# Optimization experiments

Measured on AMD Instinct MI355X. Metric: run time of the kernel, lower is better.

Reference implementation:

```python
import jax, jax.numpy as jnp
import numpy as np

B, Lq, Lk, E = 4, 512, 512, 128
D = 2 * E  # input feature dim = 2*encode_size


def setup_inputs() -> dict:
    key = jax.random.key(0)
    ks = jax.random.split(key, 6)
    return {
        "query": jax.random.normal(ks[0], (B, Lq, D), jnp.float32),
        "key": jax.random.normal(ks[1], (B, Lk, D), jnp.float32),
        "value": jax.random.normal(ks[2], (B, Lq, D), jnp.float32),
        "Wc1": jax.random.normal(ks[3], (D, E), jnp.float32) / np.sqrt(D),
        "Wc2": jax.random.normal(ks[4], (D, E), jnp.float32) / np.sqrt(D),
        "vc": jax.random.normal(ks[5], (E,), jnp.float32) / np.sqrt(E),
    }


def reference(query, key, value, Wc1, Wc2, vc):
    # q: [B, Lq, E], k: [B, Lk, E]
    q = query @ Wc1
    k = key @ Wc2
    # additive (Bahdanau) scores: tanh(q + k) reduced by vc -> [B, Lk, Lq]
    sjt = jnp.einsum('blqe,e->blq', jnp.tanh(q[:, None, :, :] + k[:, :, None, :]), vc)
    atten = jax.nn.softmax(sjt, axis=2)  # softmax over Lq (dim=2), dropout p=0.0 is identity
    context = jnp.einsum('blq,bqd->bld', atten, value)  # [B, Lk, D]
    return (context, atten)
```

## Files before the change

kernel.cpp:

```cpp
#include <hip/hip_runtime.h>

#define NB 4
#define LQ 512
#define LK 512
#define EE 128
#define DD 256

__device__ __forceinline__ float fast_rcp(float x) { return __builtin_amdgcn_rcpf(x); }

__global__ __launch_bounds__(256) void proj_exp_kernel(
    const float* __restrict__ query, const float* __restrict__ key,
    const float* __restrict__ Wc1, const float* __restrict__ Wc2,
    float* __restrict__ EqT, float* __restrict__ Ek)
{
    __shared__ float in_s[8][DD];
    const int r0 = blockIdx.x * 8;
    const bool is_q = (r0 < NB * LQ);
    const float* src = is_q ? query : key;
    const float* W   = is_q ? Wc1   : Wc2;
    const int rbase  = is_q ? r0    : r0 - NB * LQ;

    const float4* srow4 = (const float4*)(src + (size_t)rbase * DD);
    #pragma unroll
    for (int i = 0; i < 2; ++i)
        ((float4*)in_s)[i * 256 + threadIdx.x] = srow4[i * 256 + threadIdx.x];
    __syncthreads();

    const int c  = threadIdx.x & 127;
    const int rg = threadIdx.x >> 7;
    float acc[4] = {0.f, 0.f, 0.f, 0.f};
    for (int d = 0; d < DD; d += 8) {
        const float w0 = W[(d + 0) * EE + c];
        const float w1 = W[(d + 1) * EE + c];
        const float w2 = W[(d + 2) * EE + c];
        const float w3 = W[(d + 3) * EE + c];
        const float w4 = W[(d + 4) * EE + c];
        const float w5 = W[(d + 5) * EE + c];
        const float w6 = W[(d + 6) * EE + c];
        const float w7 = W[(d + 7) * EE + c];
        #pragma unroll
        for (int i = 0; i < 4; ++i) {
            const float4 xa = *(const float4*)&in_s[rg * 4 + i][d];
            const float4 xb = *(const float4*)&in_s[rg * 4 + i][d + 4];
            acc[i] += xa.x * w0 + xa.y * w1 + xa.z * w2 + xa.w * w3
                    + xb.x * w4 + xb.y * w5 + xb.z * w6 + xb.w * w7;
        }
    }
    if (is_q) {
        const int b    = rbase >> 9;
        const int qloc = (rbase & 511) + rg * 4;
        float4 o;
        o.x = __expf(2.0f * acc[0]); o.y = __expf(2.0f * acc[1]);
        o.z = __expf(2.0f * acc[2]); o.w = __expf(2.0f * acc[3]);
        *(float4*)&EqT[((size_t)(b * EE + c)) * LQ + qloc] = o;
    } else {
        #pragma unroll
        for (int i = 0; i < 4; ++i)
            Ek[(size_t)(rbase + rg * 4 + i) * EE + c] = __expf(2.0f * acc[i]);
    }
}

__global__ __launch_bounds__(512) void atten_kernel(
    const float* __restrict__ EqT, const float* __restrict__ Ek,
    const float* __restrict__ vc, float* __restrict__ attn)
{
    __shared__ float  ek_s[4][EE];
    __shared__ float  vc_s[EE];
    __shared__ float  s2p_s[3][4][LQ];
    __shared__ float  sj_s[4][LQ];
    __shared__ float2 mZ_s[4][2];
    __shared__ float  scale_s[4][2];
    const int b   = blockIdx.x >> 7;
    const int lt  = blockIdx.x & 127;
    const int l0  = lt * 4;
    const int tid = threadIdx.x;
    const int qq  = tid & 127;
    const int eg  = tid >> 7;

    ((float*)ek_s)[tid] = Ek[((size_t)b * LK + l0) * EE + tid];
    if (tid < EE) vc_s[tid] = vc[tid];
    __syncthreads();

    float vcsum = 0.f;
    #pragma unroll
    for (int e = 0; e < EE; e += 4) {
        const float4 v = *(const float4*)&vc_s[e];
        vcsum += (v.x + v.y) + (v.z + v.w);
    }

    const float4* eq4 = (const float4*)(EqT + (size_t)b * EE * LQ);
    float s2[4][4];
    #pragma unroll
    for (int l = 0; l < 4; ++l) { s2[l][0]=0.f; s2[l][1]=0.f; s2[l][2]=0.f; s2[l][3]=0.f; }

    #pragma unroll 4
    for (int i = 0; i < 32; ++i) {
        const int e = eg * 32 + i;
        const float4 a  = eq4[(size_t)e * 128 + qq];
        const float  vv = vc_s[e];
        #pragma unroll
        for (int l = 0; l < 4; ++l) {
            const float kk = ek_s[l][e];
            s2[l][0] += vv * fast_rcp(a.x * kk + 1.0f);
            s2[l][1] += vv * fast_rcp(a.y * kk + 1.0f);
            s2[l][2] += vv * fast_rcp(a.z * kk + 1.0f);
            s2[l][3] += vv * fast_rcp(a.w * kk + 1.0f);
        }
    }

    if (eg > 0) {
        #pragma unroll
        for (int l = 0; l < 4; ++l)
            *(float4*)&s2p_s[eg - 1][l][qq * 4] =
                make_float4(s2[l][0], s2[l][1], s2[l][2], s2[l][3]);
    }
    __syncthreads();
    if (eg == 0) {
        #pragma unroll
        for (int l = 0; l < 4; ++l) {
            const float4 p0 = *(const float4*)&s2p_s[0][l][qq * 4];
            const float4 p1 = *(const float4*)&s2p_s[1][l][qq * 4];
            const float4 p2 = *(const float4*)&s2p_s[2][l][qq * 4];
            float4 sj;
            sj.x = vcsum - 2.0f * (s2[l][0] + p0.x + p1.x + p2.x);
            sj.y = vcsum - 2.0f * (s2[l][1] + p0.y + p1.y + p2.y);
            sj.z = vcsum - 2.0f * (s2[l][2] + p0.z + p1.z + p2.z);
            sj.w = vcsum - 2.0f * (s2[l][3] + p0.w + p1.w + p2.w);
            *(float4*)&sj_s[l][qq * 4] = sj;
        }
    }
    __syncthreads();

    const int w = tid >> 6, lane = tid & 63;
    const int l = w & 3, h2 = w >> 2, base = h2 * 256;
    float m = -1e30f;
    #pragma unroll
    for (int i = 0; i < 4; ++i) m = fmaxf(m, sj_s[l][base + lane + 64 * i]);
    #pragma unroll
    for (int off = 32; off >= 1; off >>= 1) m = fmaxf(m, __shfl_xor(m, off));
    float Z = 0.f;
    #pragma unroll
    for (int i = 0; i < 4; ++i) {
        const int idx = base + lane + 64 * i;
        const float ex = __expf(sj_s[l][idx] - m);
        sj_s[l][idx] = ex;
        Z += ex;
    }
    #pragma unroll
    for (int off = 32; off >= 1; off >>= 1) Z += __shfl_xor(Z, off);
    if (lane == 0) mZ_s[l][h2] = make_float2(m, Z);
    __syncthreads();
    if (lane == 0) {
        const float2 A = mZ_s[l][0], B2 = mZ_s[l][1];
        const float M  = fmaxf(A.x, B2.x);
        const float Zt = A.y * __expf(A.x - M) + B2.y * __expf(B2.x - M);
        scale_s[l][h2] = __expf((h2 ? B2.x : A.x) - M) * fast_rcp(Zt);
    }
    __syncthreads();

    const int q = tid;
    #pragma unroll
    for (int li = 0; li < 4; ++li)
        attn[(size_t)(b * LK + l0 + li) * LQ + q] = sj_s[li][q] * scale_s[li][q >> 8];
}

__global__ __launch_bounds__(1024) void context_kernel(
    const float* __restrict__ attn, const float* __restrict__ value,
    float* __restrict__ ctx)
{
    const int b    = blockIdx.x >> 6;
    const int lt   = blockIdx.x & 63;
    const int row0 = b * LK + lt * 8;
    const int tid  = threadIdx.x;
    const int g    = tid >> 6;
    const int lane = tid & 63;
    const float4* v4 = (const float4*)(value + (size_t)b * LQ * DD);

    float4 ac[8];
    #pragma unroll
    for (int l = 0; l < 8; ++l) ac[l] = make_float4(0.f, 0.f, 0.f, 0.f);

    const int q0 = g * 32;
    for (int q = q0; q < q0 + 32; q += 4) {
        float4 a[8];
        #pragma unroll
        for (int l = 0; l < 8; ++l)
            a[l] = *(const float4*)(attn + (size_t)(row0 + l) * LQ + q);
        const float4 v0 = v4[(size_t)(q + 0) * 64 + lane];
        const float4 v1 = v4[(size_t)(q + 1) * 64 + lane];
        const float4 v2 = v4[(size_t)(q + 2) * 64 + lane];
        const float4 v3 = v4[(size_t)(q + 3) * 64 + lane];
        #pragma unroll
        for (int l = 0; l < 8; ++l) {
            ac[l].x += a[l].x * v0.x; ac[l].y += a[l].x * v0.y;
            ac[l].z += a[l].x * v0.z; ac[l].w += a[l].x * v0.w;
            ac[l].x += a[l].y * v1.x; ac[l].y += a[l].y * v1.y;
            ac[l].z += a[l].y * v1.z; ac[l].w += a[l].y * v1.w;
            ac[l].x += a[l].z * v2.x; ac[l].y += a[l].z * v2.y;
            ac[l].z += a[l].z * v2.z; ac[l].w += a[l].z * v2.w;
            ac[l].x += a[l].w * v3.x; ac[l].y += a[l].w * v3.y;
            ac[l].z += a[l].w * v3.z; ac[l].w += a[l].w * v3.w;
        }
    }

    __shared__ float4 red[8][8][64];
    if (g >= 8) {
        #pragma unroll
        for (int l = 0; l < 8; ++l) red[g - 8][l][lane] = ac[l];
    }
    __syncthreads();
    if (g < 8) {
        #pragma unroll
        for (int l = 0; l < 8; ++l) {
            const float4 r = red[g][l][lane];
            ac[l].x += r.x; ac[l].y += r.y; ac[l].z += r.z; ac[l].w += r.w;
        }
    }
    __syncthreads();
    if (g >= 4 && g < 8) {
        #pragma unroll
        for (int l = 0; l < 8; ++l) red[g - 4][l][lane] = ac[l];
    }
    __syncthreads();
    if (g < 4) {
        #pragma unroll
        for (int l = 0; l < 8; ++l) {
            const float4 r = red[g][l][lane];
            ac[l].x += r.x; ac[l].y += r.y; ac[l].z += r.z; ac[l].w += r.w;
        }
    }
    __syncthreads();
    if (g == 2 || g == 3) {
        #pragma unroll
        for (int l = 0; l < 8; ++l) red[g - 2][l][lane] = ac[l];
    }
    __syncthreads();
    if (g < 2) {
        #pragma unroll
        for (int l = 0; l < 8; ++l) {
            const float4 r = red[g][l][lane];
            ac[l].x += r.x; ac[l].y += r.y; ac[l].z += r.z; ac[l].w += r.w;
        }
    }
    __syncthreads();
    if (g == 1) {
        #pragma unroll
        for (int l = 0; l < 8; ++l) red[0][l][lane] = ac[l];
    }
    __syncthreads();
    if (g == 0) {
        #pragma unroll
        for (int l = 0; l < 8; ++l) {
            const float4 r = red[0][l][lane];
            ac[l].x += r.x; ac[l].y += r.y; ac[l].z += r.z; ac[l].w += r.w;
            ((float4*)ctx)[(size_t)(row0 + l) * 64 + lane] = ac[l];
        }
    }
}

extern "C" void kernel_launch(void* const* d_in, const int* in_sizes, int n_in,
                              void* d_out, int out_size, void* d_ws, size_t ws_size,
                              hipStream_t stream) {
    const float* query = (const float*)d_in[0];
    const float* key   = (const float*)d_in[1];
    const float* value = (const float*)d_in[2];
    const float* Wc1   = (const float*)d_in[3];
    const float* Wc2   = (const float*)d_in[4];
    const float* vc    = (const float*)d_in[5];

    float* ctx  = (float*)d_out;
    float* attn = (float*)d_out + (size_t)NB * LK * DD;

    float* EqT = ctx;
    float* Ek  = ctx + (size_t)NB * LQ * EE;

    proj_exp_kernel<<<dim3(512), dim3(256), 0, stream>>>(query, key, Wc1, Wc2, EqT, Ek);
    atten_kernel<<<dim3(NB * (LK / 4)), dim3(512), 0, stream>>>(EqT, Ek, vc, attn);
    context_kernel<<<dim3(NB * (LK / 8)), dim3(1024), 0, stream>>>(attn, value, ctx);
}
```

Baseline: 119.7 us.

## Fuse key projection into attention kernel and split query projection

Moves the key projection and exp into the attention kernel: each block loads its 4 key rows into shared memory and computes Ek itself, so Ek no longer goes through global memory. The projection kernel now handles only the query side, with half the grid. The launch code calls proj_q_kernel twice with identical arguments, which repeats the same work and adds an extra launch. The attention kernel also gains a serial 256-term dot product per thread reading Wc2 from global memory.

Result: slower. 140.3 us (+17.2%).

```diff
diff --git a/kernel.cpp b/kernel.cpp
--- a/kernel.cpp
+++ b/kernel.cpp
@@ -8,19 +8,14 @@
 
 __device__ __forceinline__ float fast_rcp(float x) { return __builtin_amdgcn_rcpf(x); }
 
-__global__ __launch_bounds__(256) void proj_exp_kernel(
-    const float* __restrict__ query, const float* __restrict__ key,
-    const float* __restrict__ Wc1, const float* __restrict__ Wc2,
-    float* __restrict__ EqT, float* __restrict__ Ek)
+__global__ __launch_bounds__(256) void proj_q_kernel(
+    const float* __restrict__ query, const float* __restrict__ Wc1,
+    float* __restrict__ EqT)
 {
     __shared__ float in_s[8][DD];
-    const int r0 = blockIdx.x * 8;
-    const bool is_q = (r0 < NB * LQ);
-    const float* src = is_q ? query : key;
-    const float* W   = is_q ? Wc1   : Wc2;
-    const int rbase  = is_q ? r0    : r0 - NB * LQ;
-
-    const float4* srow4 = (const float4*)(src + (size_t)rbase * DD);
+    const int rbase = blockIdx.x * 8;
+
+    const float4* srow4 = (const float4*)(query + (size_t)rbase * DD);
     #pragma unroll
     for (int i = 0; i < 2; ++i)
         ((float4*)in_s)[i * 256 + threadIdx.x] = srow4[i * 256 + threadIdx.x];
@@ -30,14 +25,14 @@
     const int rg = threadIdx.x >> 7;
     float acc[4] = {0.f, 0.f, 0.f, 0.f};
     for (int d = 0; d < DD; d += 8) {
-        const float w0 = W[(d + 0) * EE + c];
-        const float w1 = W[(d + 1) * EE + c];
-        const float w2 = W[(d + 2) * EE + c];
-        const float w3 = W[(d + 3) * EE + c];
-        const float w4 = W[(d + 4) * EE + c];
-        const float w5 = W[(d + 5) * EE + c];
-        const float w6 = W[(d + 6) * EE + c];
-        const float w7 = W[(d + 7) * EE + c];
+        const float w0 = Wc1[(d + 0) * EE + c];
+        const float w1 = Wc1[(d + 1) * EE + c];
+        const float w2 = Wc1[(d + 2) * EE + c];
+        const float w3 = Wc1[(d + 3) * EE + c];
+        const float w4 = Wc1[(d + 4) * EE + c];
+        const float w5 = Wc1[(d + 5) * EE + c];
+        const float w6 = Wc1[(d + 6) * EE + c];
+        const float w7 = Wc1[(d + 7) * EE + c];
         #pragma unroll
         for (int i = 0; i < 4; ++i) {
             const float4 xa = *(const float4*)&in_s[rg * 4 + i][d];
@@ -46,24 +41,20 @@
                     + xb.x * w4 + xb.y * w5 + xb.z * w6 + xb.w * w7;
         }
     }
-    if (is_q) {
-        const int b    = rbase >> 9;
-        const int qloc = (rbase & 511) + rg * 4;
-        float4 o;
-        o.x = __expf(2.0f * acc[0]); o.y = __expf(2.0f * acc[1]);
-        o.z = __expf(2.0f * acc[2]); o.w = __expf(2.0f * acc[3]);
-        *(float4*)&EqT[((size_t)(b * EE + c)) * LQ + qloc] = o;
-    } else {
-        #pragma unroll
-        for (int i = 0; i < 4; ++i)
-            Ek[(size_t)(rbase + rg * 4 + i) * EE + c] = __expf(2.0f * acc[i]);
-    }
+    const int b    = rbase >> 9;
+    const int qloc = (rbase & 511) + rg * 4;
+    float4 o;
+    o.x = __expf(2.0f * acc[0]); o.y = __expf(2.0f * acc[1]);
+    o.z = __expf(2.0f * acc[2]); o.w = __expf(2.0f * acc[3]);
+    *(float4*)&EqT[((size_t)(b * EE + c)) * LQ + qloc] = o;
 }
 
 __global__ __launch_bounds__(512) void atten_kernel(
-    const float* __restrict__ EqT, const float* __restrict__ Ek,
-    const float* __restrict__ vc, float* __restrict__ attn)
+    const float* __restrict__ EqT, const float* __restrict__ key,
+    const float* __restrict__ Wc2, const float* __restrict__ vc,
+    float* __restrict__ attn)
 {
+    __shared__ float  key_s[4][DD];
     __shared__ float  ek_s[4][EE];
     __shared__ float  vc_s[EE];
     __shared__ float  s2p_s[3][4][LQ];
@@ -74,11 +65,27 @@
     const int lt  = blockIdx.x & 127;
     const int l0  = lt * 4;
     const int tid = threadIdx.x;
-    const int qq  = tid & 127;
-    const int eg  = tid >> 7;
-
-    ((float*)ek_s)[tid] = Ek[((size_t)b * LK + l0) * EE + tid];
+
+    ((float2*)key_s)[tid] = ((const float2*)(key + ((size_t)b * LK + l0) * DD))[tid];
     if (tid < EE) vc_s[tid] = vc[tid];
+    __syncthreads();
+
+    {
+        const int l = tid >> 7, e = tid & 127;
+        const float* krow = key_s[l];
+        float acc = 0.f;
+        for (int d = 0; d < DD; d += 8) {
+            acc += krow[d + 0] * Wc2[(d + 0) * EE + e]
+                 + krow[d + 1] * Wc2[(d + 1) * EE + e]
+                 + krow[d + 2] * Wc2[(d + 2) * EE + e]
+                 + krow[d + 3] * Wc2[(d + 3) * EE + e]
+                 + krow[d + 4] * Wc2[(d + 4) * EE + e]
+                 + krow[d + 5] * Wc2[(d + 5) * EE + e]
+                 + krow[d + 6] * Wc2[(d + 6) * EE + e]
+                 + krow[d + 7] * Wc2[(d + 7) * EE + e];
+        }
+        ek_s[l][e] = __expf(2.0f * acc);
+    }
     __syncthreads();
 
     float vcsum = 0.f;
@@ -89,6 +96,8 @@
     }
 
     const float4* eq4 = (const float4*)(EqT + (size_t)b * EE * LQ);
+    const int qq = tid & 127;
+    const int eg = tid >> 7;
     float s2[4][4];
     #pragma unroll
     for (int l = 0; l < 4; ++l) { s2[l][0]=0.f; s2[l][1]=0.f; s2[l][2]=0.f; s2[l][3]=0.f; }
@@ -272,9 +281,9 @@
     float* attn = (float*)d_out + (size_t)NB * LK * DD;
 
     float* EqT = ctx;
-    float* Ek  = ctx + (size_t)NB * LQ * EE;
-
-    proj_exp_kernel<<<dim3(512), dim3(256), 0, stream>>>(query, key, Wc1, Wc2, EqT, Ek);
-    atten_kernel<<<dim3(NB * (LK / 4)), dim3(512), 0, stream>>>(EqT, Ek, vc, attn);
+
+    proj_q_kernel<<<dim3(256), dim3(256), 0, stream>>>(query, Wc1, EqT);
+    proj_q_kernel<<<dim3(256), dim3(256), 0, stream>>>(query, Wc1, EqT);
+    atten_kernel<<<dim3(NB * (LK / 4)), dim3(512), 0, stream>>>(EqT, key, Wc2, vc, attn);
     context_kernel<<<dim3(NB * (LK / 8)), dim3(1024), 0, stream>>>(attn, value, ctx);
 }
```
